# Performance work log

Measured on AMD Instinct MI355X. Metric: run time of the kernel, lower is better.

The kernel has to match this reference:

```python
import jax, jax.numpy as jnp
import numpy as np

B, G, S, H = 4, 8, 1024, 1024
KD = H // 8  # key_dim = hidden_dim // 8


def setup_inputs() -> dict:
    key = jax.random.key(0)
    ks = jax.random.split(key, 8)
    x = jax.random.normal(ks[0], (B, G, S, H), dtype=jnp.float32)
    inv_h = 1.0 / np.sqrt(H).astype(np.float32)
    Wq = jax.random.normal(ks[1], (H, KD), dtype=jnp.float32) * inv_h
    bq = jax.random.normal(ks[2], (KD,), dtype=jnp.float32) * 0.01
    Wk = jax.random.normal(ks[3], (H, KD), dtype=jnp.float32) * inv_h
    bk = jax.random.normal(ks[4], (KD,), dtype=jnp.float32) * 0.01
    Wv = jax.random.normal(ks[5], (H, H), dtype=jnp.float32) * inv_h
    bv = jax.random.normal(ks[6], (H,), dtype=jnp.float32) * 0.01
    gamma = jax.random.normal(ks[7], (1,), dtype=jnp.float32) * 0.1
    return {"x": x, "Wq": Wq, "bq": bq, "Wk": Wk, "bk": bk, "Wv": Wv, "bv": bv, "gamma": gamma}


def reference(x, Wq, bq, Wk, bk, Wv, bv, gamma):
    # x: [b, g, q, f]
    q = x @ Wq + bq          # [b, g, q, kd]
    k = x @ Wk + bk          # [b, g, k, kd]
    v = x @ Wv + bv          # [b, g, v, f]
    # NOTE: original forward never applies self.scale -> unscaled logits.
    att = jax.nn.softmax(jnp.einsum('bgqf,bgkf->bgqk', q, k), axis=-1)
    out = jnp.einsum('bgvf,bgqv->bgqf', v, att)
    return gamma * out + x
```

## Files before the change

### kernel.cpp

```cpp
#include <hip/hip_runtime.h>

typedef unsigned short u16;
typedef unsigned char u8;
typedef __attribute__((ext_vector_type(8))) short bf16x8;
typedef __attribute__((ext_vector_type(4))) float f32x4;
typedef __attribute__((ext_vector_type(4))) int i32x4;
typedef __attribute__((ext_vector_type(8))) int i32x8;

__device__ __forceinline__ u16 f2bf(float f) {
  unsigned u = __builtin_bit_cast(unsigned, f);
  u += 0x7fffu + ((u >> 16) & 1u);
  return (u16)(u >> 16);
}

__device__ __forceinline__ float bf2f(u16 h) {
  unsigned u = ((unsigned)h) << 16;
  return __builtin_bit_cast(float, u);
}

__device__ __forceinline__ unsigned pkbf(float lo, float hi) {
  unsigned r;
  asm("v_cvt_pk_bf16_f32 %0, %1, %2" : "=v"(r) : "v"(lo), "v"(hi));
  return r;
}

__device__ __forceinline__ void gll16(const void* g, void* l) {
  __builtin_amdgcn_global_load_lds((const __attribute__((address_space(1))) void*)g,
                                   (__attribute__((address_space(3))) void*)l, 16, 0, 0);
}

__device__ __forceinline__ f32x4 mfma_fp8_k128(i32x8 a, i32x8 b, f32x4 c) {
  return __builtin_amdgcn_mfma_scale_f32_16x16x128_f8f6f4(
      a, b, c, 0, 0, 0, 0x7f7f7f7f, 0, 0x7f7f7f7f);
}

__global__ void prep_k(const float* __restrict__ x, u16* __restrict__ xb, u8* __restrict__ xf8,
                       const float* __restrict__ Wq, const float* __restrict__ Wk,
                       const float* __restrict__ Wv, u16* __restrict__ wt, u8* __restrict__ wv8,
                       const float* __restrict__ bq, const float* __restrict__ bk,
                       const float* __restrict__ bv, float* __restrict__ bc) {
  __shared__ float tile[64][65];
  const int b = blockIdx.x;
  const int t = threadIdx.x;
  if (b < 16384) {
    const size_t i = ((size_t)b * 256 + t) * 8;
    float4 a = *(const float4*)(x + i);
    float4 c = *(const float4*)(x + i + 4);
    uint4 u;
    u.x = pkbf(a.x, a.y);
    u.y = pkbf(a.z, a.w);
    u.z = pkbf(c.x, c.y);
    u.w = pkbf(c.z, c.w);
    *(uint4*)(xb + i) = u;
    uint2 v;
    unsigned p0 = __builtin_amdgcn_cvt_pk_fp8_f32(a.x, a.y, 0, false);
    p0 = __builtin_amdgcn_cvt_pk_fp8_f32(a.z, a.w, p0, true);
    unsigned p1 = __builtin_amdgcn_cvt_pk_fp8_f32(c.x, c.y, 0, false);
    p1 = __builtin_amdgcn_cvt_pk_fp8_f32(c.z, c.w, p1, true);
    v.x = p0; v.y = p1;
    *(uint2*)(xf8 + i) = v;
  } else if (b < 16704) {
    const int tb = b - 16384;
    const int n0 = (tb % 20) * 64;
    const int f0 = (tb / 20) * 64;
    const float* src; int ld, coff;
    if (n0 < 128)      { src = Wq; ld = 128;  coff = n0; }
    else if (n0 < 256) { src = Wk; ld = 128;  coff = n0 - 128; }
    else               { src = Wv; ld = 1024; coff = n0 - 256; }
    const int r = t >> 4, c4 = (t & 15) * 4;
    #pragma unroll
    for (int i = 0; i < 4; ++i) {
      float4 v = *(const float4*)(src + (size_t)(f0 + r + 16 * i) * ld + coff + c4);
      tile[r + 16 * i][c4 + 0] = v.x;
      tile[r + 16 * i][c4 + 1] = v.y;
      tile[r + 16 * i][c4 + 2] = v.z;
      tile[r + 16 * i][c4 + 3] = v.w;
    }
    __syncthreads();
    if (n0 < 256) {
      #pragma unroll
      for (int i = 0; i < 4; ++i) {
        const int nr = r + 16 * i;
        ushort4 h;
        h.x = f2bf(tile[c4 + 0][nr]);
        h.y = f2bf(tile[c4 + 1][nr]);
        h.z = f2bf(tile[c4 + 2][nr]);
        h.w = f2bf(tile[c4 + 3][nr]);
        *(ushort4*)(wt + (size_t)(n0 + nr) * 1024 + f0 + c4) = h;
      }
    } else {
      #pragma unroll
      for (int i = 0; i < 4; ++i) {
        const int nr = r + 16 * i;
        unsigned v8 = __builtin_amdgcn_cvt_pk_fp8_f32(tile[c4 + 0][nr], tile[c4 + 1][nr], 0, false);
        v8 = __builtin_amdgcn_cvt_pk_fp8_f32(tile[c4 + 2][nr], tile[c4 + 3][nr], v8, true);
        *(unsigned*)(wv8 + (size_t)(n0 - 256 + nr) * 1024 + f0 + c4) = v8;
      }
    }
  } else {
    for (int i = t; i < 1280; i += 256)
      bc[i] = (i < 128) ? bq[i] : ((i < 256) ? bk[i - 128] : bv[i - 256]);
  }
}

__global__ __launch_bounds__(256, 2) void gemm_all_k(
    const u16* __restrict__ xb, const u16* __restrict__ wt,
    const u8* __restrict__ xf8, const u8* __restrict__ wv8,
    const float* __restrict__ bc, u16* __restrict__ qkv, u8* __restrict__ vt) {
  __shared__ char smem[32768];
  char* sAc = smem;
  char* sBc = smem + 16384;
  const int t = threadIdx.x;
  const int w = t >> 6, lane = t & 63;
  const int wr = w >> 1, wc = w & 1;
  const int lm = lane & 15, lg = lane >> 4;
  const f32x4 FZ = {0.f, 0.f, 0.f, 0.f};

  if (blockIdx.x < 512) {
    const int bid = blockIdx.x;
    const int xcd = bid & 7, g = bid >> 3;
    const int mb = xcd + 8 * (g >> 1);
    const int nt = g & 1;
    const int m0 = mb * 128;
    const int n0 = nt * 128;

    const int brow = t >> 3;
    const int bcol = 8 * ((t & 7) ^ ((t >> 3) & 7));
    const int kswz = (lm & 7) << 4;
    const u16* ab = xb + (size_t)(m0 + brow) * 1024 + bcol;
    const u16* wb = wt + (size_t)(n0 + brow) * 1024 + bcol;

    f32x4 acc[4][4];
    #pragma unroll
    for (int mi = 0; mi < 4; ++mi)
      #pragma unroll
      for (int ni = 0; ni < 4; ++ni) acc[mi][ni] = FZ;

    for (int kt = 0; kt < 16; ++kt) {
      const int k0 = kt * 64;
      char* da = sAc + w * 1024;
      char* db = sBc + w * 1024;
      #pragma unroll
      for (int i = 0; i < 4; ++i) {
        gll16(ab + (size_t)(32 * i) * 1024 + k0, da + 4096 * i);
        gll16(wb + (size_t)(32 * i) * 1024 + k0, db + 4096 * i);
      }
      __syncthreads();
      #pragma unroll
      for (int ks = 0; ks < 2; ++ks) {
        const int ka = (ks * 64 + lg * 16) ^ kswz;
        bf16x8 aF[4], bF[4];
        #pragma unroll
        for (int mi = 0; mi < 4; ++mi)
          aF[mi] = *(const bf16x8*)(sAc + (wr * 64 + mi * 16 + lm) * 128 + ka);
        #pragma unroll
        for (int ni = 0; ni < 4; ++ni)
          bF[ni] = *(const bf16x8*)(sBc + (wc * 64 + ni * 16 + lm) * 128 + ka);
        #pragma unroll
        for (int mi = 0; mi < 4; ++mi)
          #pragma unroll
          for (int ni = 0; ni < 4; ++ni)
            acc[mi][ni] = __builtin_amdgcn_mfma_f32_16x16x32_bf16(aF[mi], bF[ni], acc[mi][ni], 0, 0, 0);
      }
      __syncthreads();
    }

    #pragma unroll
    for (int ni = 0; ni < 4; ++ni) {
      const int col = n0 + wc * 64 + ni * 16 + lm;
      const float bias = bc[col];
      #pragma unroll
      for (int mi = 0; mi < 4; ++mi) {
        const int r0 = m0 + wr * 64 + mi * 16 + lg * 4;
        #pragma unroll
        for (int j = 0; j < 4; ++j)
          qkv[(size_t)(r0 + j) * 256 + col] = f2bf(acc[mi][ni][j] + bias);
      }
    }
  } else {
    const int bid = blockIdx.x - 512;
    const int xcd = bid & 7, g = bid >> 3;
    const int mb = xcd + 8 * (g >> 3);
    const int nt = g & 7;
    const int m0 = mb * 128;
    const int n0 = nt * 128;

    const int brow = t >> 3;
    const int bcol = 16 * ((t & 7) ^ ((t >> 3) & 7));
    const int kswz = (lm & 7) << 4;
    const u8* ab = xf8 + (size_t)(m0 + brow) * 1024 + bcol;
    const u8* wb = wv8 + (size_t)(n0 + brow) * 1024 + bcol;

    f32x4 acc[4][4];
    #pragma unroll
    for (int mi = 0; mi < 4; ++mi)
      #pragma unroll
      for (int ni = 0; ni < 4; ++ni) acc[mi][ni] = FZ;

    for (int kt = 0; kt < 8; ++kt) {
      const int k0 = kt * 128;
      #pragma unroll
      for (int i = 0; i < 4; ++i) {
        gll16(ab + (size_t)(32 * i) * 1024 + k0, sAc + i * 4096 + t * 16);
        gll16(wb + (size_t)(32 * i) * 1024 + k0, sBc + i * 4096 + t * 16);
      }
      __syncthreads();
      i32x8 bF[4];
      #pragma unroll
      for (int ni = 0; ni < 4; ++ni) {
        const char* rb = sBc + (wc * 64 + ni * 16 + lm) * 128;
        i32x4 lo = *(const i32x4*)(rb + ((lg * 32) ^ kswz));
        i32x4 hi = *(const i32x4*)(rb + ((lg * 32 + 16) ^ kswz));
        bF[ni] = __builtin_shufflevector(lo, hi, 0, 1, 2, 3, 4, 5, 6, 7);
      }
      #pragma unroll
      for (int mi = 0; mi < 4; ++mi) {
        const char* ra = sAc + (wr * 64 + mi * 16 + lm) * 128;
        i32x4 lo = *(const i32x4*)(ra + ((lg * 32) ^ kswz));
        i32x4 hi = *(const i32x4*)(ra + ((lg * 32 + 16) ^ kswz));
        i32x8 aF = __builtin_shufflevector(lo, hi, 0, 1, 2, 3, 4, 5, 6, 7);
        #pragma unroll
        for (int ni = 0; ni < 4; ++ni)
          acc[mi][ni] = mfma_fp8_k128(aF, bF[ni], acc[mi][ni]);
      }
      __syncthreads();
    }

    #pragma unroll
    for (int ni = 0; ni < 4; ++ni) {
      const int h = n0 + wc * 64 + ni * 16 + lm;
      const float bias = bc[256 + h];
      #pragma unroll
      for (int mi = 0; mi < 4; ++mi) {
        const int r0 = m0 + wr * 64 + mi * 16 + lg * 4;
        const int bg = r0 >> 10;
        const int sb = r0 & 1023;
        unsigned v32 = __builtin_amdgcn_cvt_pk_fp8_f32(acc[mi][ni][0] + bias,
                                                       acc[mi][ni][1] + bias, 0, false);
        v32 = __builtin_amdgcn_cvt_pk_fp8_f32(acc[mi][ni][2] + bias,
                                              acc[mi][ni][3] + bias, v32, true);
        *(unsigned*)(vt + ((size_t)(bg * 1024 + h) << 10) + sb) = v32;
      }
    }
  }
}

__global__ __launch_bounds__(512, 2) void qks_k(const u16* __restrict__ qk,
                                                u8* __restrict__ P) {
  __shared__ float smax[8][32];
  __shared__ float ssum[8][32];
  const int t = threadIdx.x;
  const int w = t >> 6, lane = t & 63;
  const int lm = lane & 15, lg = lane >> 4;
  const int bid = blockIdx.x;
  const int qt = (bid >> 3) & 31;
  const int bg = (((bid >> 8) & 3) << 3) | (bid & 7);
  const f32x4 FZ = {0.f, 0.f, 0.f, 0.f};

  bf16x8 qf[2][4];
  #pragma unroll
  for (int qc = 0; qc < 2; ++qc)
    #pragma unroll
    for (int ks = 0; ks < 4; ++ks)
      qf[qc][ks] = *(const bf16x8*)(qk +
          (size_t)(bg * 1024 + qt * 32 + qc * 16 + lm) * 256 + ks * 32 + lg * 8);

  f32x4 sc[8][2];
  #pragma unroll
  for (int ch = 0; ch < 8; ++ch) { sc[ch][0] = FZ; sc[ch][1] = FZ; }
  const u16* kbase = qk + (size_t)(bg * 1024 + w * 128) * 256 + 128;
  #pragma unroll
  for (int ch = 0; ch < 8; ++ch) {
    bf16x8 kf[4];
    #pragma unroll
    for (int ks = 0; ks < 4; ++ks)
      kf[ks] = *(const bf16x8*)(kbase + (size_t)(ch * 16 + lm) * 256 + ks * 32 + lg * 8);
    #pragma unroll
    for (int ks = 0; ks < 4; ++ks) {
      sc[ch][0] = __builtin_amdgcn_mfma_f32_16x16x32_bf16(kf[ks], qf[0][ks], sc[ch][0], 0, 0, 0);
      sc[ch][1] = __builtin_amdgcn_mfma_f32_16x16x32_bf16(kf[ks], qf[1][ks], sc[ch][1], 0, 0, 0);
    }
  }

  float mx[2];
  #pragma unroll
  for (int qc = 0; qc < 2; ++qc) {
    float m = sc[0][qc][0];
    #pragma unroll
    for (int ch = 0; ch < 8; ++ch)
      #pragma unroll
      for (int j = 0; j < 4; ++j) m = fmaxf(m, sc[ch][qc][j]);
    m = fmaxf(m, __shfl_xor(m, 16));
    m = fmaxf(m, __shfl_xor(m, 32));
    mx[qc] = m;
  }
  if (lg == 0) { smax[w][lm] = mx[0]; smax[w][16 + lm] = mx[1]; }
  __syncthreads();
  float gm[2];
  #pragma unroll
  for (int qc = 0; qc < 2; ++qc) {
    float m = smax[0][qc * 16 + lm];
    #pragma unroll
    for (int wp = 1; wp < 8; ++wp) m = fmaxf(m, smax[wp][qc * 16 + lm]);
    gm[qc] = m;
  }

  float ls[2] = {0.f, 0.f};
  #pragma unroll
  for (int ch = 0; ch < 8; ++ch)
    #pragma unroll
    for (int qc = 0; qc < 2; ++qc) {
      f32x4 e;
      #pragma unroll
      for (int j = 0; j < 4; ++j) e[j] = __expf(sc[ch][qc][j] - gm[qc]);
      sc[ch][qc] = e;
      ls[qc] += (e[0] + e[1]) + (e[2] + e[3]);
    }
  #pragma unroll
  for (int qc = 0; qc < 2; ++qc) {
    ls[qc] += __shfl_xor(ls[qc], 16);
    ls[qc] += __shfl_xor(ls[qc], 32);
  }
  if (lg == 0) { ssum[w][lm] = ls[0]; ssum[w][16 + lm] = ls[1]; }
  __syncthreads();
  float inv[2];
  #pragma unroll
  for (int qc = 0; qc < 2; ++qc) {
    float s = ssum[0][qc * 16 + lm];
    #pragma unroll
    for (int wp = 1; wp < 8; ++wp) s += ssum[wp][qc * 16 + lm];
    inv[qc] = 1.0f / s;
  }

  const int s0 = (2 * (lg & 1)) * 16 + lm;
  const int s1 = s0 + 16;
  const bool lo = (lg < 2);
  #pragma unroll
  for (int qc = 0; qc < 2; ++qc) {
    u8* pr = P + ((size_t)(bg * 1024 + qt * 32 + qc * 16 + lm) << 10) + w * 128 + lg * 8;
    #pragma unroll
    for (int c = 0; c < 4; ++c) {
      unsigned ue = __builtin_amdgcn_cvt_pk_fp8_f32(sc[2 * c][qc][0] * inv[qc],
                                                    sc[2 * c][qc][1] * inv[qc], 0, false);
      ue = __builtin_amdgcn_cvt_pk_fp8_f32(sc[2 * c][qc][2] * inv[qc],
                                           sc[2 * c][qc][3] * inv[qc], ue, true);
      unsigned uo = __builtin_amdgcn_cvt_pk_fp8_f32(sc[2 * c + 1][qc][0] * inv[qc],
                                                    sc[2 * c + 1][qc][1] * inv[qc], 0, false);
      uo = __builtin_amdgcn_cvt_pk_fp8_f32(sc[2 * c + 1][qc][2] * inv[qc],
                                           sc[2 * c + 1][qc][3] * inv[qc], uo, true);
      unsigned e0 = __shfl(ue, s0), o0 = __shfl(uo, s0);
      unsigned e1 = __shfl(ue, s1), o1 = __shfl(uo, s1);
      uint2 pw;
      pw.x = lo ? e0 : o0;
      pw.y = lo ? e1 : o1;
      *(uint2*)(pr + c * 32) = pw;
    }
  }
}

__global__ __launch_bounds__(256, 2) void pv_k(
    const u8* __restrict__ P, const u8* __restrict__ vt,
    const u16* __restrict__ xb, const float* __restrict__ gam,
    float* __restrict__ out) {
  __shared__ u8 sA[128 * 128];
  __shared__ u8 sB[128 * 128];
  char* sAc = (char*)sA;
  char* sBc = (char*)sB;
  const int t = threadIdx.x;
  const int w = t >> 6, lane = t & 63;
  const int wr = w >> 1, wc = w & 1;
  const int lm = lane & 15, lg = lane >> 4;
  const int bid = blockIdx.x;
  const int bg = (((bid >> 9) & 3) << 3) | (bid & 7);
  const int qb = (bid >> 6) & 7;
  const int hb = (bid >> 3) & 7;
  const int m0 = qb * 128, n0 = hb * 128;
  const f32x4 FZ = {0.f, 0.f, 0.f, 0.f};

  const int brow = t >> 3;
  const int bcol = 16 * ((t & 7) ^ ((t >> 3) & 7));
  const int kswz = (lm & 7) << 4;
  const u8* pb = P + ((size_t)(bg * 1024 + m0 + brow) << 10) + bcol;
  const u8* wb = vt + ((size_t)(bg * 1024 + n0 + brow) << 10) + bcol;

  f32x4 acc[4][4];
  #pragma unroll
  for (int mi = 0; mi < 4; ++mi)
    #pragma unroll
    for (int ni = 0; ni < 4; ++ni) acc[mi][ni] = FZ;

  for (int kt = 0; kt < 8; ++kt) {
    const int k0 = kt * 128;
    #pragma unroll
    for (int i = 0; i < 4; ++i) {
      gll16(pb + (size_t)(32 * i) * 1024 + k0, sAc + i * 4096 + t * 16);
      gll16(wb + (size_t)(32 * i) * 1024 + k0, sBc + i * 4096 + t * 16);
    }
    __syncthreads();
    i32x8 bF[4];
    #pragma unroll
    for (int ni = 0; ni < 4; ++ni) {
      const char* rb = sBc + (wc * 64 + ni * 16 + lm) * 128;
      i32x4 lo = *(const i32x4*)(rb + ((lg * 32) ^ kswz));
      i32x4 hi = *(const i32x4*)(rb + ((lg * 32 + 16) ^ kswz));
      bF[ni] = __builtin_shufflevector(lo, hi, 0, 1, 2, 3, 4, 5, 6, 7);
    }
    #pragma unroll
    for (int mi = 0; mi < 4; ++mi) {
      const char* ra = sAc + (wr * 64 + mi * 16 + lm) * 128;
      i32x4 lo = *(const i32x4*)(ra + ((lg * 32) ^ kswz));
      i32x4 hi = *(const i32x4*)(ra + ((lg * 32 + 16) ^ kswz));
      i32x8 aF = __builtin_shufflevector(lo, hi, 0, 1, 2, 3, 4, 5, 6, 7);
      #pragma unroll
      for (int ni = 0; ni < 4; ++ni)
        acc[mi][ni] = mfma_fp8_k128(aF, bF[ni], acc[mi][ni]);
    }
    __syncthreads();
  }

  const float g0 = gam[0];
  #pragma unroll
  for (int mi = 0; mi < 4; ++mi)
    #pragma unroll
    for (int j = 0; j < 4; ++j) {
      const size_t row = (size_t)(bg * 1024 + m0 + wr * 64 + mi * 16 + lg * 4 + j);
      #pragma unroll
      for (int ni = 0; ni < 4; ++ni) {
        const int col = n0 + wc * 64 + ni * 16 + lm;
        const size_t idx = row * 1024 + col;
        __builtin_nontemporal_store(g0 * acc[mi][ni][j] + bf2f(xb[idx]), &out[idx]);
      }
    }
}

extern "C" void kernel_launch(void* const* d_in, const int* in_sizes, int n_in,
                              void* d_out, int out_size, void* d_ws, size_t ws_size,
                              hipStream_t stream) {
  const float* x  = (const float*)d_in[0];
  const float* Wq = (const float*)d_in[1];
  const float* bq = (const float*)d_in[2];
  const float* Wk = (const float*)d_in[3];
  const float* bk = (const float*)d_in[4];
  const float* Wv = (const float*)d_in[5];
  const float* bv = (const float*)d_in[6];
  const float* gm = (const float*)d_in[7];
  float* out = (float*)d_out;

  char* ws = (char*)d_ws;
  u16*   wt  = (u16*)(ws);
  float* bc  = (float*)(ws + 524288);
  u16*   qk  = (u16*)(ws + 529408);
  u8*    vt  = (u8*)(ws + 17306624);
  u8*    Pm  = (u8*)(ws + 50861056);
  u16*   xb  = (u16*)(ws + 84415488);
  u8*    xf8 = (u8*)(ws + 151524352);
  u8*    wv8 = (u8*)(ws + 185078784);

  prep_k<<<16705, 256, 0, stream>>>(x, xb, xf8, Wq, Wk, Wv, wt, wv8, bq, bk, bv, bc);
  gemm_all_k<<<dim3(2560), 256, 0, stream>>>(xb, wt, xf8, wv8, bc, qk, vt);
  qks_k<<<dim3(1024), 512, 0, stream>>>(qk, Pm);
  pv_k<<<dim3(2048), 256, 0, stream>>>(Pm, vt, xb, gm, out);
}
```

Before: 217.2 us.

## Split QK projection and co-schedule V projection with QK^T softmax blocks

The combined projection kernel is split. The Q/K projection now runs alone as its own kernel. The V projection GEMM is fused into one launch with the QK^T softmax work, with even and odd blocks alternating between the two tasks. The softmax path is reshaped from 512-thread blocks covering 32 query rows to 256-thread blocks covering 16 query rows, so the two block types share a launch shape. The aim is to overlap the compute-bound V GEMM with the latency-bound softmax and cut one dependency stage, at the cost of more register pressure per softmax wave and a mixed workload in one launch.

```diff
diff --git a/kernel.cpp b/kernel.cpp
--- a/kernel.cpp
+++ b/kernel.cpp
@@ -103,83 +103,96 @@
   }
 }
 
-__global__ __launch_bounds__(256, 2) void gemm_all_k(
+__global__ __launch_bounds__(256, 2) void gemm_qk_k(
     const u16* __restrict__ xb, const u16* __restrict__ wt,
-    const u8* __restrict__ xf8, const u8* __restrict__ wv8,
-    const float* __restrict__ bc, u16* __restrict__ qkv, u8* __restrict__ vt) {
-  __shared__ char smem[32768];
-  char* sAc = smem;
-  char* sBc = smem + 16384;
+    const float* __restrict__ bc, u16* __restrict__ qkv) {
+  __shared__ u16 sA[128 * 64];
+  __shared__ u16 sB[128 * 64];
+  char* sAc = (char*)sA;
+  char* sBc = (char*)sB;
   const int t = threadIdx.x;
   const int w = t >> 6, lane = t & 63;
   const int wr = w >> 1, wc = w & 1;
   const int lm = lane & 15, lg = lane >> 4;
+  const int bid = blockIdx.x;
+  const int xcd = bid & 7, g = bid >> 3;
+  const int mb = xcd + 8 * (g >> 1);
+  const int nt = g & 1;
+  const int m0 = mb * 128;
+  const int n0 = nt * 128;
   const f32x4 FZ = {0.f, 0.f, 0.f, 0.f};
 
-  if (blockIdx.x < 512) {
-    const int bid = blockIdx.x;
-    const int xcd = bid & 7, g = bid >> 3;
-    const int mb = xcd + 8 * (g >> 1);
-    const int nt = g & 1;
-    const int m0 = mb * 128;
-    const int n0 = nt * 128;
-
-    const int brow = t >> 3;
-    const int bcol = 8 * ((t & 7) ^ ((t >> 3) & 7));
-    const int kswz = (lm & 7) << 4;
-    const u16* ab = xb + (size_t)(m0 + brow) * 1024 + bcol;
-    const u16* wb = wt + (size_t)(n0 + brow) * 1024 + bcol;
-
-    f32x4 acc[4][4];
-    #pragma unroll
-    for (int mi = 0; mi < 4; ++mi)
-      #pragma unroll
-      for (int ni = 0; ni < 4; ++ni) acc[mi][ni] = FZ;
-
-    for (int kt = 0; kt < 16; ++kt) {
-      const int k0 = kt * 64;
-      char* da = sAc + w * 1024;
-      char* db = sBc + w * 1024;
-      #pragma unroll
-      for (int i = 0; i < 4; ++i) {
-        gll16(ab + (size_t)(32 * i) * 1024 + k0, da + 4096 * i);
-        gll16(wb + (size_t)(32 * i) * 1024 + k0, db + 4096 * i);
-      }
-      __syncthreads();
-      #pragma unroll
-      for (int ks = 0; ks < 2; ++ks) {
-        const int ka = (ks * 64 + lg * 16) ^ kswz;
-        bf16x8 aF[4], bF[4];
-        #pragma unroll
-        for (int mi = 0; mi < 4; ++mi)
-          aF[mi] = *(const bf16x8*)(sAc + (wr * 64 + mi * 16 + lm) * 128 + ka);
+  const int brow = t >> 3;
+  const int bcol = 8 * ((t & 7) ^ ((t >> 3) & 7));
+  const int kswz = (lm & 7) << 4;
+  const u16* ab = xb + (size_t)(m0 + brow) * 1024 + bcol;
+  const u16* wb = wt + (size_t)(n0 + brow) * 1024 + bcol;
+
+  f32x4 acc[4][4];
+  #pragma unroll
+  for (int mi = 0; mi < 4; ++mi)
+    #pragma unroll
+    for (int ni = 0; ni < 4; ++ni) acc[mi][ni] = FZ;
+
+  for (int kt = 0; kt < 16; ++kt) {
+    const int k0 = kt * 64;
+    char* da = sAc + w * 1024;
+    char* db = sBc + w * 1024;
+    #pragma unroll
+    for (int i = 0; i < 4; ++i) {
+      gll16(ab + (size_t)(32 * i) * 1024 + k0, da + 4096 * i);
+      gll16(wb + (size_t)(32 * i) * 1024 + k0, db + 4096 * i);
+    }
+    __syncthreads();
+    #pragma unroll
+    for (int ks = 0; ks < 2; ++ks) {
+      const int ka = (ks * 64 + lg * 16) ^ kswz;
+      bf16x8 aF[4], bF[4];
+      #pragma unroll
+      for (int mi = 0; mi < 4; ++mi)
+        aF[mi] = *(const bf16x8*)(sAc + (wr * 64 + mi * 16 + lm) * 128 + ka);
+      #pragma unroll
+      for (int ni = 0; ni < 4; ++ni)
+        bF[ni] = *(const bf16x8*)(sBc + (wc * 64 + ni * 16 + lm) * 128 + ka);
+      #pragma unroll
+      for (int mi = 0; mi < 4; ++mi)
         #pragma unroll
         for (int ni = 0; ni < 4; ++ni)
-          bF[ni] = *(const bf16x8*)(sBc + (wc * 64 + ni * 16 + lm) * 128 + ka);
-        #pragma unroll
-        for (int mi = 0; mi < 4; ++mi)
-          #pragma unroll
-          for (int ni = 0; ni < 4; ++ni)
-            acc[mi][ni] = __builtin_amdgcn_mfma_f32_16x16x32_bf16(aF[mi], bF[ni], acc[mi][ni], 0, 0, 0);
-      }
-      __syncthreads();
-    }
-
-    #pragma unroll
-    for (int ni = 0; ni < 4; ++ni) {
-      const int col = n0 + wc * 64 + ni * 16 + lm;
-      const float bias = bc[col];
-      #pragma unroll
-      for (int mi = 0; mi < 4; ++mi) {
-        const int r0 = m0 + wr * 64 + mi * 16 + lg * 4;
-        #pragma unroll
-        for (int j = 0; j < 4; ++j)
-          qkv[(size_t)(r0 + j) * 256 + col] = f2bf(acc[mi][ni][j] + bias);
-      }
-    }
-  } else {
-    const int bid = blockIdx.x - 512;
-    const int xcd = bid & 7, g = bid >> 3;
+          acc[mi][ni] = __builtin_amdgcn_mfma_f32_16x16x32_bf16(aF[mi], bF[ni], acc[mi][ni], 0, 0, 0);
+    }
+    __syncthreads();
+  }
+
+  #pragma unroll
+  for (int ni = 0; ni < 4; ++ni) {
+    const int col = n0 + wc * 64 + ni * 16 + lm;
+    const float bias = bc[col];
+    #pragma unroll
+    for (int mi = 0; mi < 4; ++mi) {
+      const int r0 = m0 + wr * 64 + mi * 16 + lg * 4;
+      #pragma unroll
+      for (int j = 0; j < 4; ++j)
+        qkv[(size_t)(r0 + j) * 256 + col] = f2bf(acc[mi][ni][j] + bias);
+    }
+  }
+}
+
+__global__ __launch_bounds__(256, 2) void vqs_k(
+    const u8* __restrict__ xf8, const u8* __restrict__ wv8,
+    const float* __restrict__ bc, u8* __restrict__ vt,
+    const u16* __restrict__ qk, u8* __restrict__ P) {
+  __shared__ char smem[32768];
+  const int t = threadIdx.x;
+  const int w = t >> 6, lane = t & 63;
+  const int lm = lane & 15, lg = lane >> 4;
+  const f32x4 FZ = {0.f, 0.f, 0.f, 0.f};
+  const int sub = blockIdx.x >> 1;
+
+  if ((blockIdx.x & 1) == 0) {
+    char* sAc = smem;
+    char* sBc = smem + 16384;
+    const int wr = w >> 1, wc = w & 1;
+    const int xcd = sub & 7, g = sub >> 3;
     const int mb = xcd + 8 * (g >> 3);
     const int nt = g & 7;
     const int m0 = mb * 128;
@@ -242,112 +255,69 @@
         *(unsigned*)(vt + ((size_t)(bg * 1024 + h) << 10) + sb) = v32;
       }
     }
-  }
-}
-
-__global__ __launch_bounds__(512, 2) void qks_k(const u16* __restrict__ qk,
-                                                u8* __restrict__ P) {
-  __shared__ float smax[8][32];
-  __shared__ float ssum[8][32];
-  const int t = threadIdx.x;
-  const int w = t >> 6, lane = t & 63;
-  const int lm = lane & 15, lg = lane >> 4;
-  const int bid = blockIdx.x;
-  const int qt = (bid >> 3) & 31;
-  const int bg = (((bid >> 8) & 3) << 3) | (bid & 7);
-  const f32x4 FZ = {0.f, 0.f, 0.f, 0.f};
-
-  bf16x8 qf[2][4];
-  #pragma unroll
-  for (int qc = 0; qc < 2; ++qc)
+  } else {
+    float* smax = (float*)smem;
+    float* ssum = (float*)(smem + 256);
+    const int bg = ((sub >> 9) & 3) * 8 + (sub & 7);
+    const int qt = (sub >> 3) & 63;
+
+    bf16x8 qf[4];
     #pragma unroll
     for (int ks = 0; ks < 4; ++ks)
-      qf[qc][ks] = *(const bf16x8*)(qk +
-          (size_t)(bg * 1024 + qt * 32 + qc * 16 + lm) * 256 + ks * 32 + lg * 8);
-
-  f32x4 sc[8][2];
-  #pragma unroll
-  for (int ch = 0; ch < 8; ++ch) { sc[ch][0] = FZ; sc[ch][1] = FZ; }
-  const u16* kbase = qk + (size_t)(bg * 1024 + w * 128) * 256 + 128;
-  #pragma unroll
-  for (int ch = 0; ch < 8; ++ch) {
-    bf16x8 kf[4];
-    #pragma unroll
-    for (int ks = 0; ks < 4; ++ks)
-      kf[ks] = *(const bf16x8*)(kbase + (size_t)(ch * 16 + lm) * 256 + ks * 32 + lg * 8);
-    #pragma unroll
-    for (int ks = 0; ks < 4; ++ks) {
-      sc[ch][0] = __builtin_amdgcn_mfma_f32_16x16x32_bf16(kf[ks], qf[0][ks], sc[ch][0], 0, 0, 0);
-      sc[ch][1] = __builtin_amdgcn_mfma_f32_16x16x32_bf16(kf[ks], qf[1][ks], sc[ch][1], 0, 0, 0);
-    }
-  }
-
-  float mx[2];
-  #pragma unroll
-  for (int qc = 0; qc < 2; ++qc) {
-    float m = sc[0][qc][0];
-    #pragma unroll
-    for (int ch = 0; ch < 8; ++ch)
-      #pragma unroll
-      for (int j = 0; j < 4; ++j) m = fmaxf(m, sc[ch][qc][j]);
+      qf[ks] = *(const bf16x8*)(qk +
+          (size_t)(bg * 1024 + qt * 16 + lm) * 256 + ks * 32 + lg * 8);
+
+    f32x4 sc[16];
+    #pragma unroll
+    for (int ch = 0; ch < 16; ++ch) sc[ch] = FZ;
+    const u16* kbase = qk + (size_t)(bg * 1024 + w * 256) * 256 + 128;
+    #pragma unroll
+    for (int ch = 0; ch < 16; ++ch) {
+      bf16x8 kf[4];
+      #pragma unroll
+      for (int ks = 0; ks < 4; ++ks)
+        kf[ks] = *(const bf16x8*)(kbase + (size_t)(ch * 16 + lm) * 256 + ks * 32 + lg * 8);
+      #pragma unroll
+      for (int ks = 0; ks < 4; ++ks)
+        sc[ch] = __builtin_amdgcn_mfma_f32_16x16x32_bf16(kf[ks], qf[ks], sc[ch], 0, 0, 0);
+    }
+
+    float m = sc[0][0];
+    #pragma unroll
+    for (int ch = 0; ch < 16; ++ch)
+      #pragma unroll
+      for (int j = 0; j < 4; ++j) m = fmaxf(m, sc[ch][j]);
     m = fmaxf(m, __shfl_xor(m, 16));
     m = fmaxf(m, __shfl_xor(m, 32));
-    mx[qc] = m;
-  }
-  if (lg == 0) { smax[w][lm] = mx[0]; smax[w][16 + lm] = mx[1]; }
-  __syncthreads();
-  float gm[2];
-  #pragma unroll
-  for (int qc = 0; qc < 2; ++qc) {
-    float m = smax[0][qc * 16 + lm];
-    #pragma unroll
-    for (int wp = 1; wp < 8; ++wp) m = fmaxf(m, smax[wp][qc * 16 + lm]);
-    gm[qc] = m;
-  }
-
-  float ls[2] = {0.f, 0.f};
-  #pragma unroll
-  for (int ch = 0; ch < 8; ++ch)
-    #pragma unroll
-    for (int qc = 0; qc < 2; ++qc) {
+    if (lg == 0) smax[w * 16 + lm] = m;
+    __syncthreads();
+    float gm = fmaxf(fmaxf(smax[lm], smax[16 + lm]), fmaxf(smax[32 + lm], smax[48 + lm]));
+
+    float ls = 0.f;
+    #pragma unroll
+    for (int ch = 0; ch < 16; ++ch) {
       f32x4 e;
       #pragma unroll
-      for (int j = 0; j < 4; ++j) e[j] = __expf(sc[ch][qc][j] - gm[qc]);
-      sc[ch][qc] = e;
-      ls[qc] += (e[0] + e[1]) + (e[2] + e[3]);
-    }
-  #pragma unroll
-  for (int qc = 0; qc < 2; ++qc) {
-    ls[qc] += __shfl_xor(ls[qc], 16);
-    ls[qc] += __shfl_xor(ls[qc], 32);
-  }
-  if (lg == 0) { ssum[w][lm] = ls[0]; ssum[w][16 + lm] = ls[1]; }
-  __syncthreads();
-  float inv[2];
-  #pragma unroll
-  for (int qc = 0; qc < 2; ++qc) {
-    float s = ssum[0][qc * 16 + lm];
-    #pragma unroll
-    for (int wp = 1; wp < 8; ++wp) s += ssum[wp][qc * 16 + lm];
-    inv[qc] = 1.0f / s;
-  }
-
-  const int s0 = (2 * (lg & 1)) * 16 + lm;
-  const int s1 = s0 + 16;
-  const bool lo = (lg < 2);
-  #pragma unroll
-  for (int qc = 0; qc < 2; ++qc) {
-    u8* pr = P + ((size_t)(bg * 1024 + qt * 32 + qc * 16 + lm) << 10) + w * 128 + lg * 8;
-    #pragma unroll
-    for (int c = 0; c < 4; ++c) {
-      unsigned ue = __builtin_amdgcn_cvt_pk_fp8_f32(sc[2 * c][qc][0] * inv[qc],
-                                                    sc[2 * c][qc][1] * inv[qc], 0, false);
-      ue = __builtin_amdgcn_cvt_pk_fp8_f32(sc[2 * c][qc][2] * inv[qc],
-                                           sc[2 * c][qc][3] * inv[qc], ue, true);
-      unsigned uo = __builtin_amdgcn_cvt_pk_fp8_f32(sc[2 * c + 1][qc][0] * inv[qc],
-                                                    sc[2 * c + 1][qc][1] * inv[qc], 0, false);
-      uo = __builtin_amdgcn_cvt_pk_fp8_f32(sc[2 * c + 1][qc][2] * inv[qc],
-                                           sc[2 * c + 1][qc][3] * inv[qc], uo, true);
+      for (int j = 0; j < 4; ++j) e[j] = __expf(sc[ch][j] - gm);
+      sc[ch] = e;
+      ls += (e[0] + e[1]) + (e[2] + e[3]);
+    }
+    ls += __shfl_xor(ls, 16);
+    ls += __shfl_xor(ls, 32);
+    if (lg == 0) ssum[w * 16 + lm] = ls;
+    __syncthreads();
+    const float inv = 1.0f / (((ssum[lm] + ssum[16 + lm]) + (ssum[32 + lm] + ssum[48 + lm])));
+
+    const int s0 = (2 * (lg & 1)) * 16 + lm;
+    const int s1 = s0 + 16;
+    const bool lo = (lg < 2);
+    u8* pr = P + ((size_t)(bg * 1024 + qt * 16 + lm) << 10) + w * 256 + lg * 8;
+    #pragma unroll
+    for (int c = 0; c < 8; ++c) {
+      unsigned ue = __builtin_amdgcn_cvt_pk_fp8_f32(sc[2 * c][0] * inv, sc[2 * c][1] * inv, 0, false);
+      ue = __builtin_amdgcn_cvt_pk_fp8_f32(sc[2 * c][2] * inv, sc[2 * c][3] * inv, ue, true);
+      unsigned uo = __builtin_amdgcn_cvt_pk_fp8_f32(sc[2 * c + 1][0] * inv, sc[2 * c + 1][1] * inv, 0, false);
+      uo = __builtin_amdgcn_cvt_pk_fp8_f32(sc[2 * c + 1][2] * inv, sc[2 * c + 1][3] * inv, uo, true);
       unsigned e0 = __shfl(ue, s0), o0 = __shfl(uo, s0);
       unsigned e1 = __shfl(ue, s1), o1 = __shfl(uo, s1);
       uint2 pw;
@@ -457,7 +427,7 @@
   u8*    wv8 = (u8*)(ws + 185078784);
 
   prep_k<<<16705, 256, 0, stream>>>(x, xb, xf8, Wq, Wk, Wv, wt, wv8, bq, bk, bv, bc);
-  gemm_all_k<<<dim3(2560), 256, 0, stream>>>(xb, wt, xf8, wv8, bc, qk, vt);
-  qks_k<<<dim3(1024), 512, 0, stream>>>(qk, Pm);
+  gemm_qk_k<<<dim3(512), 256, 0, stream>>>(xb, wt, bc, qk);
+  vqs_k<<<dim3(4096), 256, 0, stream>>>(xf8, wv8, bc, vt, qk, Pm);
   pv_k<<<dim3(2048), 256, 0, stream>>>(Pm, vt, xb, gm, out);
 }
```

Result: slower. 255.9 us (+17.8%).
